# Kernel optimization log

Measured on AMD Instinct MI355X. Metric: run time of the kernel, lower is better.

Reference implementation:

```python
import jax, jax.numpy as jnp
import numpy as np

EMBED_DIM = 256
NUM_HEADS = 8
HEAD_DIM = EMBED_DIM // NUM_HEADS
ADJ_CHANNELS = 4
B, N = 8, 1024


def setup_inputs() -> dict:
    key = jax.random.key(0)
    ks = jax.random.split(key, 12)
    s = 1.0 / np.sqrt(EMBED_DIM)
    sa = 1.0 / np.sqrt(ADJ_CHANNELS)
    return {
        "x": jax.random.normal(ks[0], (B, N, EMBED_DIM), dtype=jnp.float32),
        "adj": jax.random.uniform(ks[1], (B, N, N, ADJ_CHANNELS), dtype=jnp.float32),
        "Wq": jax.random.uniform(ks[2], (EMBED_DIM, EMBED_DIM), jnp.float32, -s, s),
        "bq": jnp.zeros((EMBED_DIM,), jnp.float32),
        "Wk": jax.random.uniform(ks[3], (EMBED_DIM, EMBED_DIM), jnp.float32, -s, s),
        "bk": jnp.zeros((EMBED_DIM,), jnp.float32),
        "Wv": jax.random.uniform(ks[4], (EMBED_DIM, EMBED_DIM), jnp.float32, -s, s),
        "bv": jnp.zeros((EMBED_DIM,), jnp.float32),
        "Wo": jax.random.uniform(ks[5], (EMBED_DIM, EMBED_DIM), jnp.float32, -s, s),
        "bo": jnp.zeros((EMBED_DIM,), jnp.float32),
        "Wa": jax.random.uniform(ks[6], (ADJ_CHANNELS, NUM_HEADS), jnp.float32, -sa, sa),
        "ba": jnp.zeros((NUM_HEADS,), jnp.float32),
    }


def reference(x, adj, Wq, bq, Wk, bk, Wv, bv, Wo, bo, Wa, ba):
    Bs, Ns, E = x.shape
    H, D = NUM_HEADS, HEAD_DIM
    def heads(W, b):
        return (x @ W + b).reshape(Bs, Ns, H, D).transpose(0, 2, 1, 3)  # [B,H,N,D]
    Q, K, V = heads(Wq, bq), heads(Wk, bk), heads(Wv, bv)
    # adjacency-derived additive bias: [B,N,N,C] -> [B,N,N,H] -> [B,H,N,N]
    bias = jnp.moveaxis(adj @ Wa + ba, -1, 1)
    scores = jnp.einsum("bhnd,bhmd->bhnm", Q, K) / np.sqrt(D) + bias
    attn = jax.nn.softmax(scores, axis=-1)
    ctx = jnp.einsum("bhnm,bhmd->bhnd", attn, V)  # [B,H,N,D]
    ctx = ctx.transpose(0, 2, 1, 3).reshape(Bs, Ns, E)
    return ctx @ Wo + bo + x
```

## Files before the change

kernel.cpp:

```cpp
#include <hip/hip_runtime.h>
#include <hip/hip_bf16.h>

#define BATCH 8
#define SEQ   1024
#define EMB   256
#define NH    8
#define HD    32
#define QSCALE 0.2550030053f

typedef __attribute__((ext_vector_type(8))) short short8;
typedef __attribute__((ext_vector_type(4))) float floatx4;

__device__ __forceinline__ ushort f2bf(float f) {
    __hip_bfloat16 h = __float2bfloat16(f);
    return *reinterpret_cast<ushort*>(&h);
}
__device__ __forceinline__ unsigned int pack2bf(float lo, float hi) {
    return (unsigned int)f2bf(lo) | ((unsigned int)f2bf(hi) << 16);
}

__device__ __forceinline__ void gload_lds16(const float4* g, float4* l) {
    __builtin_amdgcn_global_load_lds(
        (const __attribute__((address_space(1))) unsigned int*)g,
        (__attribute__((address_space(3))) unsigned int*)l, 16, 0, 0);
}

__global__ __launch_bounds__(256) void prep_kernel(
    const float* __restrict__ Wq, const float* __restrict__ Wk,
    const float* __restrict__ Wv, const float* __restrict__ Wo,
    ushort* __restrict__ Wqt, ushort* __restrict__ Wkt,
    ushort* __restrict__ Wvt, ushort* __restrict__ Wot)
{
    __shared__ float tilebuf[32][33];
    const int blk = blockIdx.x;
    const int mat = blk >> 6, tile = blk & 63;
    const int ti = tile >> 3, tj = tile & 7;
    const float* W = (mat == 0) ? Wq : (mat == 1) ? Wk : (mat == 2) ? Wv : Wo;
    ushort* Wt = (mat == 0) ? Wqt : (mat == 1) ? Wkt : (mat == 2) ? Wvt : Wot;
    const float scale = (mat == 0) ? QSCALE : 1.0f;

    const int tx = threadIdx.x & 31, ty = threadIdx.x >> 5;
    #pragma unroll
    for (int p = 0; p < 4; ++p)
        tilebuf[ty + p * 8][tx] = W[(size_t)(ti * 32 + ty + p * 8) * EMB + tj * 32 + tx];
    __syncthreads();
    #pragma unroll
    for (int p = 0; p < 4; ++p)
        Wt[(size_t)(tj * 32 + ty + p * 8) * EMB + ti * 32 + tx] =
            f2bf(tilebuf[tx][ty + p * 8] * scale);
}

__global__ __launch_bounds__(256) void qkv_gemm(
    const float* __restrict__ x,
    const ushort* __restrict__ Wqt, const ushort* __restrict__ Wkt,
    const ushort* __restrict__ Wvt,
    const float* __restrict__ bq, const float* __restrict__ bk,
    const float* __restrict__ bv,
    ushort* __restrict__ Qb, ushort* __restrict__ Kb, ushort* __restrict__ Vt)
{
    const int mat = blockIdx.y;
    const ushort* __restrict__ Wt = (mat == 0) ? Wqt : (mat == 1) ? Wkt : Wvt;
    const float* __restrict__ bias = (mat == 0) ? bq : (mat == 1) ? bk : bv;
    const float bscale = (mat == 0) ? QSCALE : 1.0f;

    const int w = threadIdx.x >> 6, lane = threadIdx.x & 63;
    const int quad = lane >> 4, l16 = lane & 15;
    const int row0 = blockIdx.x * 64 + w * 16;

    floatx4 acc[16];
    #pragma unroll
    for (int i = 0; i < 16; ++i) acc[i] = (floatx4){0.f, 0.f, 0.f, 0.f};

    const float* __restrict__ xrow = x + (size_t)(row0 + l16) * EMB + quad * 8;

    #pragma unroll
    for (int ks = 0; ks < 8; ++ks) {
        const float4 xa0 = *(const float4*)(xrow + ks * 32);
        const float4 xa1 = *(const float4*)(xrow + ks * 32 + 4);
        ushort au[8] = {f2bf(xa0.x), f2bf(xa0.y), f2bf(xa0.z), f2bf(xa0.w),
                        f2bf(xa1.x), f2bf(xa1.y), f2bf(xa1.z), f2bf(xa1.w)};
        const short8 a = *(const short8*)au;
        #pragma unroll
        for (int i = 0; i < 16; ++i) {
            const short8 bf = *(const short8*)(Wt + (size_t)(i * 16 + l16) * EMB + ks * 32 + quad * 8);
            acc[i] = __builtin_amdgcn_mfma_f32_16x16x32_bf16(a, bf, acc[i], 0, 0, 0);
        }
    }

    const int gr0 = row0 + quad * 4;
    if (mat < 2) {
        ushort* __restrict__ dst = (mat == 0) ? Qb : Kb;
        #pragma unroll
        for (int i = 0; i < 16; ++i) {
            const int c = i * 16 + l16, h = c >> 5, d = c & (HD - 1);
            const float bb = bias[c] * bscale;
            #pragma unroll
            for (int r = 0; r < 4; ++r) {
                const int gr = gr0 + r, b = gr >> 10, n = gr & (SEQ - 1);
                dst[((size_t)(b * NH + h) * SEQ + n) * HD + d] = f2bf(acc[i][r] + bb);
            }
        }
    } else {
        const int b = gr0 >> 10, n0 = gr0 & (SEQ - 1);
        #pragma unroll
        for (int i = 0; i < 16; ++i) {
            const int c = i * 16 + l16, h = c >> 5, d = c & (HD - 1);
            const float bb = bias[c];
            ushort4 t4;
            t4.x = f2bf(acc[i][0] + bb); t4.y = f2bf(acc[i][1] + bb);
            t4.z = f2bf(acc[i][2] + bb); t4.w = f2bf(acc[i][3] + bb);
            *(ushort4*)(Vt + ((size_t)(b * NH + h) * HD + d) * SEQ + n0) = t4;
        }
    }
}

__global__ __launch_bounds__(512, 8) void attn_kernel(
    const ushort* __restrict__ Qb, const ushort* __restrict__ Kb,
    const ushort* __restrict__ Vt, const float* __restrict__ adj,
    const float* __restrict__ Wa, const float* __restrict__ ba,
    float* __restrict__ cp, float* __restrict__ lsum)
{
    __shared__ float4 Atile[2][16][65];
    const int tid = threadIdx.x, h = tid >> 6, lane = tid & 63;
    const int quad = lane >> 4, l16 = lane & 15;
    const int q0 = blockIdx.x * 16, b = blockIdx.y, z = blockIdx.z;
    const int bh = b * NH + h;
    const int kz = z * 512;

    const float LOG2E = 1.4426950408889634f;
    const float wa0 = Wa[0 * NH + h] * LOG2E, wa1 = Wa[1 * NH + h] * LOG2E;
    const float wa2 = Wa[2 * NH + h] * LOG2E, wa3 = Wa[3 * NH + h] * LOG2E;
    const float bah = ba[h] * LOG2E;

    const short8 aq = *(const short8*)(Qb + ((size_t)bh * SEQ + q0 + l16) * HD + quad * 8);

    floatx4 o0 = {0.f, 0.f, 0.f, 0.f}, o1 = {0.f, 0.f, 0.f, 0.f};
    float lacc = 0.f;

    const float4* __restrict__ adjb = (const float4*)adj + (size_t)b * SEQ * SEQ;
    const float4* __restrict__ asrc0 = adjb + (size_t)(q0 + 2 * h)     * SEQ + kz + lane;
    const float4* __restrict__ asrc1 = adjb + (size_t)(q0 + 2 * h + 1) * SEQ + kz + lane;

    const ushort* __restrict__ Kbase = Kb + (size_t)bh * SEQ * HD + (size_t)l16 * HD + quad * 8;
    const ushort* __restrict__ Vb0 = Vt + ((size_t)bh * HD + l16) * SEQ + quad * 8;
    const ushort* __restrict__ Vb1 = Vt + ((size_t)bh * HD + 16 + l16) * SEQ + quad * 8;

    const int laneA = l16 | ((quad & 1) << 5);
    const int laneB = laneA + 16;
    const bool lowsel = quad < 2;

    gload_lds16(asrc0, &Atile[0][2 * h][0]);
    gload_lds16(asrc1, &Atile[0][2 * h + 1][0]);
    __syncthreads();

    for (int it = 0; it < 8; ++it) {
        const int cur = it & 1;
        if (it < 7) {
            gload_lds16(asrc0 + (it + 1) * 64, &Atile[cur ^ 1][2 * h][0]);
            gload_lds16(asrc1 + (it + 1) * 64, &Atile[cur ^ 1][2 * h + 1][0]);
        }
        const int key0 = kz + it * 64;

        #pragma unroll
        for (int c = 0; c < 2; ++c) {
            const int kc = key0 + c * 32;
            const short8 ka = *(const short8*)(Kbase + (size_t)kc * HD);
            const short8 kb = *(const short8*)(Kbase + (size_t)(kc + 16) * HD);
            const floatx4 zz = {0.f, 0.f, 0.f, 0.f};
            floatx4 sA = __builtin_amdgcn_mfma_f32_16x16x32_bf16(ka, aq, zz, 0, 0, 0);
            floatx4 sB = __builtin_amdgcn_mfma_f32_16x16x32_bf16(kb, aq, zz, 0, 0, 0);

            float pA[4], pB[4];
            #pragma unroll
            for (int r = 0; r < 4; ++r) {
                const int col = c * 32 + 4 * quad + r;
                const float4 a0 = Atile[cur][l16][col];
                const float4 a1 = Atile[cur][l16][col + 16];
                const float b0 = fmaf(a0.x, wa0, fmaf(a0.y, wa1, fmaf(a0.z, wa2, fmaf(a0.w, wa3, bah))));
                const float b1 = fmaf(a1.x, wa0, fmaf(a1.y, wa1, fmaf(a1.z, wa2, fmaf(a1.w, wa3, bah))));
                pA[r] = exp2f(sA[r] + b0);
                pB[r] = exp2f(sB[r] + b1);
                lacc += pA[r] + pB[r];
            }
            const unsigned int d0 = pack2bf(pA[0], pA[1]);
            const unsigned int d1 = pack2bf(pA[2], pA[3]);
            const unsigned int d2 = pack2bf(pB[0], pB[1]);
            const unsigned int d3 = pack2bf(pB[2], pB[3]);
            const int t0A = __shfl((int)d0, laneA, 64);
            const int t2A = __shfl((int)d2, laneA, 64);
            const int t1A = __shfl((int)d1, laneA, 64);
            const int t3A = __shfl((int)d3, laneA, 64);
            const int t0B = __shfl((int)d0, laneB, 64);
            const int t2B = __shfl((int)d2, laneB, 64);
            const int t1B = __shfl((int)d1, laneB, 64);
            const int t3B = __shfl((int)d3, laneB, 64);
            int4 rr;
            rr.x = lowsel ? t0A : t2A;
            rr.y = lowsel ? t1A : t3A;
            rr.z = lowsel ? t0B : t2B;
            rr.w = lowsel ? t1B : t3B;
            const short8 bp = __builtin_bit_cast(short8, rr);

            const short8 va0 = *(const short8*)(Vb0 + kc);
            const short8 va1 = *(const short8*)(Vb1 + kc);
            o0 = __builtin_amdgcn_mfma_f32_16x16x32_bf16(va0, bp, o0, 0, 0, 0);
            o1 = __builtin_amdgcn_mfma_f32_16x16x32_bf16(va1, bp, o1, 0, 0, 0);
        }
        __syncthreads();
    }

    lacc += __shfl_xor(lacc, 16, 64);
    lacc += __shfl_xor(lacc, 32, 64);

    float* __restrict__ cpz = cp + (size_t)z * BATCH * SEQ * EMB;
    float* __restrict__ lsz = lsum + (size_t)z * BATCH * SEQ * NH;
    const size_t grow = (size_t)b * SEQ + q0 + l16;
    #pragma unroll
    for (int r = 0; r < 4; ++r) {
        cpz[grow * EMB + h * HD + quad * 4 + r]      = o0[r];
        cpz[grow * EMB + h * HD + 16 + quad * 4 + r] = o1[r];
    }
    if (lane < 16)
        lsz[((size_t)b * SEQ + q0 + lane) * NH + h] = lacc;
}

__global__ __launch_bounds__(256) void outproj_gemm(
    const float* __restrict__ cp, const float* __restrict__ lsum,
    const ushort* __restrict__ Wot, const float* __restrict__ bo,
    const float* __restrict__ x, float* __restrict__ out)
{
    const int w = threadIdx.x >> 6, lane = threadIdx.x & 63;
    const int quad = lane >> 4, l16 = lane & 15;
    const int row0 = blockIdx.x * 64 + w * 16;
    const int arow = row0 + l16;
    const float* __restrict__ cp1 = cp + (size_t)BATCH * SEQ * EMB;
    const float* __restrict__ l1  = lsum + (size_t)BATCH * SEQ * NH;

    floatx4 acc[16];
    #pragma unroll
    for (int i = 0; i < 16; ++i) acc[i] = (floatx4){0.f, 0.f, 0.f, 0.f};

    #pragma unroll
    for (int ks = 0; ks < 8; ++ks) {
        const float invl = 1.0f / (lsum[(size_t)arow * NH + ks] + l1[(size_t)arow * NH + ks]);
        const size_t cb = (size_t)arow * EMB + ks * 32 + quad * 8;
        const float4 c00 = *(const float4*)(cp + cb);
        const float4 c01 = *(const float4*)(cp + cb + 4);
        const float4 c10 = *(const float4*)(cp1 + cb);
        const float4 c11 = *(const float4*)(cp1 + cb + 4);
        ushort au[8] = {
            f2bf((c00.x + c10.x) * invl), f2bf((c00.y + c10.y) * invl),
            f2bf((c00.z + c10.z) * invl), f2bf((c00.w + c10.w) * invl),
            f2bf((c01.x + c11.x) * invl), f2bf((c01.y + c11.y) * invl),
            f2bf((c01.z + c11.z) * invl), f2bf((c01.w + c11.w) * invl)};
        const short8 a = *(const short8*)au;
        #pragma unroll
        for (int i = 0; i < 16; ++i) {
            const short8 bfr = *(const short8*)(Wot + (size_t)(i * 16 + l16) * EMB + ks * 32 + quad * 8);
            acc[i] = __builtin_amdgcn_mfma_f32_16x16x32_bf16(a, bfr, acc[i], 0, 0, 0);
        }
    }

    const int gr0 = row0 + quad * 4;
    #pragma unroll
    for (int i = 0; i < 16; ++i) {
        const int c = i * 16 + l16;
        const float bov = bo[c];
        #pragma unroll
        for (int r = 0; r < 4; ++r) {
            const size_t idx = (size_t)(gr0 + r) * EMB + c;
            out[idx] = acc[i][r] + bov + x[idx];
        }
    }
}

extern "C" void kernel_launch(void* const* d_in, const int* in_sizes, int n_in,
                              void* d_out, int out_size, void* d_ws, size_t ws_size,
                              hipStream_t stream) {
    const float* x   = (const float*)d_in[0];
    const float* adj = (const float*)d_in[1];
    const float* Wq  = (const float*)d_in[2];
    const float* bq  = (const float*)d_in[3];
    const float* Wk  = (const float*)d_in[4];
    const float* bk  = (const float*)d_in[5];
    const float* Wv  = (const float*)d_in[6];
    const float* bv  = (const float*)d_in[7];
    const float* Wo  = (const float*)d_in[8];
    const float* bo  = (const float*)d_in[9];
    const float* Wa  = (const float*)d_in[10];
    const float* ba  = (const float*)d_in[11];

    const size_t per = (size_t)BATCH * NH * SEQ * HD;
    ushort* Qb  = (ushort*)d_ws;
    ushort* Kb  = Qb + per;
    ushort* Vt  = Kb + per;
    ushort* Wqt = Vt + per;
    ushort* Wkt = Wqt + EMB * EMB;
    ushort* Wvt = Wkt + EMB * EMB;
    ushort* Wot = Wvt + EMB * EMB;
    float*  cp  = (float*)(Wot + EMB * EMB);
    float*  ls  = cp + 2 * (size_t)BATCH * SEQ * EMB;

    prep_kernel<<<256, 256, 0, stream>>>(Wq, Wk, Wv, Wo, Wqt, Wkt, Wvt, Wot);
    qkv_gemm<<<dim3(BATCH * SEQ / 64, 3), 256, 0, stream>>>(
        x, Wqt, Wkt, Wvt, bq, bk, bv, Qb, Kb, Vt);
    attn_kernel<<<dim3(SEQ / 16, BATCH, 2), 512, 0, stream>>>(
        Qb, Kb, Vt, adj, Wa, ba, cp, ls);
    outproj_gemm<<<BATCH * SEQ / 64, 256, 0, stream>>>(
        cp, ls, Wot, bo, x, (float*)d_out);
}
```

Baseline: 313.0 us.

## Compute adjacency bias with MFMA via transposed bf16 LDS tile and transpose partial outputs

The adjacency bias projection moves off scalar FMAs onto MFMA. Each adj tile is converted to bf16 and transposed into a second LDS buffer, then multiplied against a block-diagonal Wa fragment and accumulated directly into the score MFMA. The adj tile loses its double buffer and gains an extra barrier per iteration, and float-to-bf16 packing switches to truncation via byte perm. Partial context outputs are now stored transposed (d-major over sequence), so the output projection reads them with strided loads, and bf16 rounding of adj and Wa changes numerics.

After: 306.2 us. 1.02x faster.

```diff
diff --git a/kernel.cpp b/kernel.cpp
--- a/kernel.cpp
+++ b/kernel.cpp
@@ -15,8 +15,10 @@
     __hip_bfloat16 h = __float2bfloat16(f);
     return *reinterpret_cast<ushort*>(&h);
 }
-__device__ __forceinline__ unsigned int pack2bf(float lo, float hi) {
-    return (unsigned int)f2bf(lo) | ((unsigned int)f2bf(hi) << 16);
+__device__ __forceinline__ unsigned int packtrunc(float lo, float hi) {
+    return __builtin_amdgcn_perm(__builtin_bit_cast(unsigned int, hi),
+                                 __builtin_bit_cast(unsigned int, lo),
+                                 0x07060302u);
 }
 
 __device__ __forceinline__ void gload_lds16(const float4* g, float4* l) {
@@ -120,7 +122,8 @@
     const float* __restrict__ Wa, const float* __restrict__ ba,
     float* __restrict__ cp, float* __restrict__ lsum)
 {
-    __shared__ float4 Atile[2][16][65];
+    __shared__ float4  Atile[16][65];
+    __shared__ ushort  AbT[64][88];
     const int tid = threadIdx.x, h = tid >> 6, lane = tid & 63;
     const int quad = lane >> 4, l16 = lane & 15;
     const int q0 = blockIdx.x * 16, b = blockIdx.y, z = blockIdx.z;
@@ -128,9 +131,28 @@
     const int kz = z * 512;
 
     const float LOG2E = 1.4426950408889634f;
-    const float wa0 = Wa[0 * NH + h] * LOG2E, wa1 = Wa[1 * NH + h] * LOG2E;
-    const float wa2 = Wa[2 * NH + h] * LOG2E, wa3 = Wa[3 * NH + h] * LOG2E;
+    ushort wab[4];
+    #pragma unroll
+    for (int c = 0; c < 4; ++c) wab[c] = f2bf(Wa[c * NH + h] * LOG2E);
+    ushort wdv0[8] = {0,0,0,0,0,0,0,0}, wdv1[8] = {0,0,0,0,0,0,0,0};
+    if (l16 == 2 * quad) {
+        #pragma unroll
+        for (int c = 0; c < 4; ++c) wdv0[c] = wab[c];
+    } else if (l16 == 2 * quad + 1) {
+        #pragma unroll
+        for (int c = 0; c < 4; ++c) wdv0[4 + c] = wab[c];
+    }
+    if (l16 == 8 + 2 * quad) {
+        #pragma unroll
+        for (int c = 0; c < 4; ++c) wdv1[c] = wab[c];
+    } else if (l16 == 9 + 2 * quad) {
+        #pragma unroll
+        for (int c = 0; c < 4; ++c) wdv1[4 + c] = wab[c];
+    }
+    const short8 wd0 = *(const short8*)wdv0;
+    const short8 wd1 = *(const short8*)wdv1;
     const float bah = ba[h] * LOG2E;
+    const floatx4 cinit = {bah, bah, bah, bah};
 
     const short8 aq = *(const short8*)(Qb + ((size_t)bh * SEQ + q0 + l16) * HD + quad * 8);
 
@@ -149,43 +171,54 @@
     const int laneB = laneA + 16;
     const bool lowsel = quad < 2;
 
-    gload_lds16(asrc0, &Atile[0][2 * h][0]);
-    gload_lds16(asrc1, &Atile[0][2 * h + 1][0]);
+    const int cq = tid & 15, ckp = tid >> 4;
+
+    gload_lds16(asrc0, &Atile[2 * h][0]);
+    gload_lds16(asrc1, &Atile[2 * h + 1][0]);
     __syncthreads();
 
     for (int it = 0; it < 8; ++it) {
-        const int cur = it & 1;
+        {
+            const float4 a0 = Atile[cq][2 * ckp];
+            const float4 a1 = Atile[cq][2 * ckp + 1];
+            uint2 w0, w1;
+            w0.x = packtrunc(a0.x, a0.y); w0.y = packtrunc(a0.z, a0.w);
+            w1.x = packtrunc(a1.x, a1.y); w1.y = packtrunc(a1.z, a1.w);
+            *(uint2*)&AbT[2 * ckp][4 * cq]     = w0;
+            *(uint2*)&AbT[2 * ckp + 1][4 * cq] = w1;
+        }
+        __syncthreads();
+
         if (it < 7) {
-            gload_lds16(asrc0 + (it + 1) * 64, &Atile[cur ^ 1][2 * h][0]);
-            gload_lds16(asrc1 + (it + 1) * 64, &Atile[cur ^ 1][2 * h + 1][0]);
+            gload_lds16(asrc0 + (it + 1) * 64, &Atile[2 * h][0]);
+            gload_lds16(asrc1 + (it + 1) * 64, &Atile[2 * h + 1][0]);
         }
         const int key0 = kz + it * 64;
 
         #pragma unroll
         for (int c = 0; c < 2; ++c) {
             const int kc = key0 + c * 32;
-            const short8 ka = *(const short8*)(Kbase + (size_t)kc * HD);
-            const short8 kb = *(const short8*)(Kbase + (size_t)(kc + 16) * HD);
-            const floatx4 zz = {0.f, 0.f, 0.f, 0.f};
-            floatx4 sA = __builtin_amdgcn_mfma_f32_16x16x32_bf16(ka, aq, zz, 0, 0, 0);
-            floatx4 sB = __builtin_amdgcn_mfma_f32_16x16x32_bf16(kb, aq, zz, 0, 0, 0);
-
             float pA[4], pB[4];
             #pragma unroll
-            for (int r = 0; r < 4; ++r) {
-                const int col = c * 32 + 4 * quad + r;
-                const float4 a0 = Atile[cur][l16][col];
-                const float4 a1 = Atile[cur][l16][col + 16];
-                const float b0 = fmaf(a0.x, wa0, fmaf(a0.y, wa1, fmaf(a0.z, wa2, fmaf(a0.w, wa3, bah))));
-                const float b1 = fmaf(a1.x, wa0, fmaf(a1.y, wa1, fmaf(a1.z, wa2, fmaf(a1.w, wa3, bah))));
-                pA[r] = exp2f(sA[r] + b0);
-                pB[r] = exp2f(sB[r] + b1);
-                lacc += pA[r] + pB[r];
+            for (int g = 0; g < 2; ++g) {
+                const int krow = c * 32 + g * 16 + l16;
+                const short8 ab1 = *(const short8*)&AbT[krow][quad * 8];
+                const short8 ab2 = *(const short8*)&AbT[krow][32 + quad * 8];
+                floatx4 bias = __builtin_amdgcn_mfma_f32_16x16x32_bf16(ab1, wd0, cinit, 0, 0, 0);
+                bias = __builtin_amdgcn_mfma_f32_16x16x32_bf16(ab2, wd1, bias, 0, 0, 0);
+                const short8 kA = *(const short8*)(Kbase + (size_t)(kc + g * 16) * HD);
+                const floatx4 s = __builtin_amdgcn_mfma_f32_16x16x32_bf16(kA, aq, bias, 0, 0, 0);
+                float* p = g ? pB : pA;
+                #pragma unroll
+                for (int r = 0; r < 4; ++r) {
+                    p[r] = exp2f(s[r]);
+                    lacc += p[r];
+                }
             }
-            const unsigned int d0 = pack2bf(pA[0], pA[1]);
-            const unsigned int d1 = pack2bf(pA[2], pA[3]);
-            const unsigned int d2 = pack2bf(pB[0], pB[1]);
-            const unsigned int d3 = pack2bf(pB[2], pB[3]);
+            const unsigned int d0 = packtrunc(pA[0], pA[1]);
+            const unsigned int d1 = packtrunc(pA[2], pA[3]);
+            const unsigned int d2 = packtrunc(pB[0], pB[1]);
+            const unsigned int d3 = packtrunc(pB[2], pB[3]);
             const int t0A = __shfl((int)d0, laneA, 64);
             const int t2A = __shfl((int)d2, laneA, 64);
             const int t1A = __shfl((int)d1, laneA, 64);
@@ -212,13 +245,12 @@
     lacc += __shfl_xor(lacc, 16, 64);
     lacc += __shfl_xor(lacc, 32, 64);
 
-    float* __restrict__ cpz = cp + (size_t)z * BATCH * SEQ * EMB;
+    float* __restrict__ cpz = cp + (size_t)z * BATCH * NH * HD * SEQ;
     float* __restrict__ lsz = lsum + (size_t)z * BATCH * SEQ * NH;
-    const size_t grow = (size_t)b * SEQ + q0 + l16;
     #pragma unroll
     for (int r = 0; r < 4; ++r) {
-        cpz[grow * EMB + h * HD + quad * 4 + r]      = o0[r];
-        cpz[grow * EMB + h * HD + 16 + quad * 4 + r] = o1[r];
+        cpz[((size_t)bh * HD + quad * 4 + r) * SEQ + q0 + l16]      = o0[r];
+        cpz[((size_t)bh * HD + 16 + quad * 4 + r) * SEQ + q0 + l16] = o1[r];
     }
     if (lane < 16)
         lsz[((size_t)b * SEQ + q0 + lane) * NH + h] = lacc;
@@ -233,7 +265,8 @@
     const int quad = lane >> 4, l16 = lane & 15;
     const int row0 = blockIdx.x * 64 + w * 16;
     const int arow = row0 + l16;
-    const float* __restrict__ cp1 = cp + (size_t)BATCH * SEQ * EMB;
+    const int b = arow >> 10, n = arow & (SEQ - 1);
+    const float* __restrict__ cp1 = cp + (size_t)BATCH * NH * HD * SEQ;
     const float* __restrict__ l1  = lsum + (size_t)BATCH * SEQ * NH;
 
     floatx4 acc[16];
@@ -243,16 +276,13 @@
     #pragma unroll
     for (int ks = 0; ks < 8; ++ks) {
         const float invl = 1.0f / (lsum[(size_t)arow * NH + ks] + l1[(size_t)arow * NH + ks]);
-        const size_t cb = (size_t)arow * EMB + ks * 32 + quad * 8;
-        const float4 c00 = *(const float4*)(cp + cb);
-        const float4 c01 = *(const float4*)(cp + cb + 4);
-        const float4 c10 = *(const float4*)(cp1 + cb);
-        const float4 c11 = *(const float4*)(cp1 + cb + 4);
-        ushort au[8] = {
-            f2bf((c00.x + c10.x) * invl), f2bf((c00.y + c10.y) * invl),
-            f2bf((c00.z + c10.z) * invl), f2bf((c00.w + c10.w) * invl),
-            f2bf((c01.x + c11.x) * invl), f2bf((c01.y + c11.y) * invl),
-            f2bf((c01.z + c11.z) * invl), f2bf((c01.w + c11.w) * invl)};
+        const size_t dbase = ((size_t)(b * NH + ks) * HD + quad * 8) * SEQ + n;
+        ushort au[8];
+        #pragma unroll
+        for (int j = 0; j < 8; ++j) {
+            const float v = cp[dbase + (size_t)j * SEQ] + cp1[dbase + (size_t)j * SEQ];
+            au[j] = f2bf(v * invl);
+        }
         const short8 a = *(const short8*)au;
         #pragma unroll
         for (int i = 0; i < 16; ++i) {
@@ -299,7 +329,7 @@
     ushort* Wvt = Wkt + EMB * EMB;
     ushort* Wot = Wvt + EMB * EMB;
     float*  cp  = (float*)(Wot + EMB * EMB);
-    float*  ls  = cp + 2 * (size_t)BATCH * SEQ * EMB;
+    float*  ls  = cp + 2 * per;
 
     prep_kernel<<<256, 256, 0, stream>>>(Wq, Wk, Wv, Wo, Wqt, Wkt, Wvt, Wot);
     qkv_gemm<<<dim3(BATCH * SEQ / 64, 3), 256, 0, stream>>>(
```
